# Optimization experiments

Measured on AMD Instinct MI355X. Metric: run time of the kernel, lower is better.

Reference implementation:

```python
import jax, jax.numpy as jnp
import numpy as np

D_MODEL = 1024
N_HEAD = 16
ATT_DIM = D_MODEL // N_HEAD  # 64
B, S = 8, 2048


def setup_inputs() -> dict:
    key = jax.random.key(0)
    kq, kk, kv, kwq, kwk, kwv = jax.random.split(key, 6)
    # xavier_uniform bound for Linear(hidden_dim -> att_dim)
    bound = float(np.sqrt(6.0 / (D_MODEL + ATT_DIM)))
    return {
        "q": jax.random.normal(kq, (B, S, D_MODEL), dtype=jnp.float32),
        "k": jax.random.normal(kk, (B, S, D_MODEL), dtype=jnp.float32),
        "v": jax.random.normal(kv, (B, S, D_MODEL), dtype=jnp.float32),
        "Wq": jax.random.uniform(kwq, (ATT_DIM, D_MODEL), jnp.float32, -bound, bound),
        "Wk": jax.random.uniform(kwk, (ATT_DIM, D_MODEL), jnp.float32, -bound, bound),
        "Wv": jax.random.uniform(kwv, (ATT_DIM, D_MODEL), jnp.float32, -bound, bound),
    }


def reference(q, k, v, Wq, Wk, Wv):
    # Linear projections (no bias): [B,S,d_model] @ [d_model,att_dim]
    qp = jnp.einsum('bsd,ed->bse', q, Wq)
    kp = jnp.einsum('bsd,ed->bse', k, Wk)
    vp = jnp.einsum('bsd,ed->bse', v, Wv)
    # Scores: note original divides by att_dim (not sqrt)
    scores = jnp.einsum('bqe,bke->bqk', qp, kp) / ATT_DIM
    probs = jax.nn.softmax(scores, axis=-1)  # [B,S,S]
    att = jnp.einsum('bqk,bke->bqe', probs, vp)  # [B,S,att_dim]
    # dropout is identity in eval mode
    return (att, probs)
```

## Files before the change

### kernel.cpp

```cpp
#include <hip/hip_runtime.h>
#include <hip/hip_bf16.h>

#define D_MODEL 1024
#define ATT_DIM 64
#define BATCH 8
#define SEQ 2048
#define MROWS (BATCH * SEQ)

typedef short bf16x8 __attribute__((ext_vector_type(8)));
typedef float f32x4 __attribute__((ext_vector_type(4)));
typedef long lx2 __attribute__((ext_vector_type(2)));

#define MFMA16(a, b, c) __builtin_amdgcn_mfma_f32_16x16x32_bf16((a), (b), (c), 0, 0, 0)

__device__ inline short f2bf(float f) {
    union { __hip_bfloat16 h; short s; } u;
    u.h = __float2bfloat16(f);
    return u.s;
}

__device__ __forceinline__ unsigned cvtpk(float lo, float hi) {
    unsigned r;
    asm("v_cvt_pk_bf16_f32 %0, %1, %2" : "=v"(r) : "v"(lo), "v"(hi));
    return r;
}

__device__ __forceinline__ void gload_lds16(const float* g, float* l) {
    __builtin_amdgcn_global_load_lds(
        (const __attribute__((address_space(1))) void*)g,
        (__attribute__((address_space(3))) void*)l, 16, 0, 0);
}

__global__ __launch_bounds__(256) void wcvt_kernel(
    const float* __restrict__ Wq, const float* __restrict__ Wk,
    const float* __restrict__ Wv, short* __restrict__ Wbf)
{
    const int idx = blockIdx.x * 256 + threadIdx.x;
    const int per = ATT_DIM * D_MODEL;
    const int base = idx * 8;
    const int mi = base / per;
    const int off = base - mi * per;
    const float* src = (mi == 0) ? Wq : (mi == 1 ? Wk : Wv);
    const float sc = (mi == 0) ? (1.0f / 64.0f) : 1.0f;
    const float4 a = *reinterpret_cast<const float4*>(src + off);
    const float4 b = *reinterpret_cast<const float4*>(src + off + 4);
    bf16x8 r;
    r[0] = f2bf(a.x * sc); r[1] = f2bf(a.y * sc);
    r[2] = f2bf(a.z * sc); r[3] = f2bf(a.w * sc);
    r[4] = f2bf(b.x * sc); r[5] = f2bf(b.y * sc);
    r[6] = f2bf(b.z * sc); r[7] = f2bf(b.w * sc);
    *reinterpret_cast<bf16x8*>(Wbf + base) = r;
}

__global__ __launch_bounds__(256) void proj_mfma_kernel(
    const float* __restrict__ q, const float* __restrict__ k,
    const float* __restrict__ v, const short* __restrict__ Wbf,
    short* __restrict__ qp, short* __restrict__ kp, short* __restrict__ vpT)
{
    const int mat = blockIdx.y;
    const float* x = (mat == 0) ? q : (mat == 1 ? k : v);
    const short* W = Wbf + mat * ATT_DIM * D_MODEL;

    __shared__ float As[2][4096];

    const int tid = threadIdx.x;
    const int w = tid >> 6;
    const int l = tid & 63;
    const int lr = l & 15;
    const int g = l >> 4;

    const int m0 = blockIdx.x * 64;
    const int row = w * 16 + lr;
    const int xr = (row & 7) << 4;

    f32x4 acc[4] = {};

    #define STAGE(c, buf)                                                      \
        {                                                                      \
            const int kt_ = (c) * 64;                                          \
            _Pragma("unroll")                                                  \
            for (int j = 0; j < 4; ++j) {                                      \
                const int rs = (w * 4 + j) * 4 + g;                            \
                const int scb = (lr * 16) ^ ((rs & 7) << 4);                   \
                gload_lds16(x + (long)(m0 + rs) * D_MODEL + kt_ + (scb >> 2),  \
                            &As[buf][(w * 4 + j) * 256]);                      \
            }                                                                  \
        }

    #define WFRAG(c, ks, ef)                                                   \
        (*reinterpret_cast<const bf16x8*>(                                     \
            W + ((ef) * 16 + lr) * D_MODEL + (c) * 64 + (ks) * 32 + g * 8))

    bf16x8 wreg[8];
    #pragma unroll
    for (int ks = 0; ks < 2; ++ks)
        #pragma unroll
        for (int ef = 0; ef < 4; ++ef) wreg[ks * 4 + ef] = WFRAG(0, ks, ef);

    STAGE(0, 0);
    __syncthreads();

    for (int c = 0; c < 16; ++c) {
        const int buf = c & 1;
        bf16x8 wnext[8];
        if (c < 15) {
            STAGE(c + 1, buf ^ 1);
            #pragma unroll
            for (int ks = 0; ks < 2; ++ks)
                #pragma unroll
                for (int ef = 0; ef < 4; ++ef)
                    wnext[ks * 4 + ef] = WFRAG(c + 1, ks, ef);
        }

        const char* Ab = (const char*)&As[buf][0] + row * 256;
        #pragma unroll
        for (int ks = 0; ks < 2; ++ks) {
            const int b0 = ks * 128 + g * 32;
            const float4 a0 = *reinterpret_cast<const float4*>(Ab + (b0 ^ xr));
            const float4 a1 = *reinterpret_cast<const float4*>(Ab + ((b0 + 16) ^ xr));
            bf16x8 af;
            af[0] = f2bf(a0.x); af[1] = f2bf(a0.y); af[2] = f2bf(a0.z); af[3] = f2bf(a0.w);
            af[4] = f2bf(a1.x); af[5] = f2bf(a1.y); af[6] = f2bf(a1.z); af[7] = f2bf(a1.w);
            #pragma unroll
            for (int ef = 0; ef < 4; ++ef)
                acc[ef] = MFMA16(af, wreg[ks * 4 + ef], acc[ef]);
        }
        __syncthreads();
        if (c < 15) {
            #pragma unroll
            for (int i = 0; i < 8; ++i) wreg[i] = wnext[i];
        }
    }
    #undef STAGE
    #undef WFRAG

    if (mat < 2) {
        short* out = (mat == 0) ? qp : kp;
        #pragma unroll
        for (int ef = 0; ef < 4; ++ef)
            #pragma unroll
            for (int j = 0; j < 4; ++j)
                out[(long)(m0 + w * 16 + g * 4 + j) * ATT_DIM + ef * 16 + lr] =
                    f2bf(acc[ef][j]);
    } else {
        const int b = m0 / SEQ;
        const int s0 = (m0 - b * SEQ) + w * 16;
        #pragma unroll
        for (int ef = 0; ef < 4; ++ef)
            #pragma unroll
            for (int j = 0; j < 4; ++j)
                vpT[((long)b * ATT_DIM + ef * 16 + lr) * SEQ + s0 + g * 4 + j] =
                    f2bf(acc[ef][j]);
    }
}

union AttnSmem {
    short pk[8][16][40];
    float o[8][64][17];
};

__global__ __launch_bounds__(512) void attn_kernel(
    const short* __restrict__ qp, const short* __restrict__ kp,
    const short* __restrict__ vpT, float* __restrict__ probs,
    float* __restrict__ att)
{
    __shared__ __align__(16) AttnSmem u;
    __shared__ float stats_m[8][16];
    __shared__ float stats_l[8][16];

    const int tid = threadIdx.x;
    const int w = tid >> 6;
    const int l = tid & 63;
    const int lr = l & 15;
    const int g = l >> 4;

    const int b = blockIdx.y;
    const int q0 = blockIdx.x * 16;

    const short* qpb = qp + ((long)b * SEQ + q0) * ATT_DIM;
    const short* kpb = kp + (long)b * SEQ * ATT_DIM;
    const short* vTb = vpT + (long)b * ATT_DIM * SEQ;

    const bf16x8 qa0 = *reinterpret_cast<const bf16x8*>(qpb + lr * ATT_DIM + g * 8);
    const bf16x8 qa1 = *reinterpret_cast<const bf16x8*>(qpb + lr * ATT_DIM + 32 + g * 8);

    const int kbeg = w * 256;

    f32x4 s[8][2];
    #pragma unroll
    for (int ch = 0; ch < 8; ++ch) {
        const short* kb = kpb + (long)(kbeg + ch * 32) * ATT_DIM;
        const bf16x8 kb00 = *reinterpret_cast<const bf16x8*>(kb + lr * ATT_DIM + g * 8);
        const bf16x8 kb01 = *reinterpret_cast<const bf16x8*>(kb + lr * ATT_DIM + 32 + g * 8);
        const bf16x8 kb10 = *reinterpret_cast<const bf16x8*>(kb + (16 + lr) * ATT_DIM + g * 8);
        const bf16x8 kb11 = *reinterpret_cast<const bf16x8*>(kb + (16 + lr) * ATT_DIM + 32 + g * 8);
        f32x4 t0 = {}; t0 = MFMA16(kb00, qa0, t0); t0 = MFMA16(kb01, qa1, t0);
        f32x4 t1 = {}; t1 = MFMA16(kb10, qa0, t1); t1 = MFMA16(kb11, qa1, t1);
        s[ch][0] = t0; s[ch][1] = t1;
    }

    float mw = -1e30f;
    #pragma unroll
    for (int ch = 0; ch < 8; ++ch)
        #pragma unroll
        for (int h = 0; h < 2; ++h)
            mw = fmaxf(mw, fmaxf(fmaxf(s[ch][h][0], s[ch][h][1]),
                                 fmaxf(s[ch][h][2], s[ch][h][3])));
    mw = fmaxf(mw, __shfl_xor(mw, 16));
    mw = fmaxf(mw, __shfl_xor(mw, 32));

    float lw = 0.f;
    #pragma unroll
    for (int ch = 0; ch < 8; ++ch)
        #pragma unroll
        for (int h = 0; h < 2; ++h)
            #pragma unroll
            for (int j = 0; j < 4; ++j) {
                const float e = __expf(s[ch][h][j] - mw);
                s[ch][h][j] = e;
                lw += e;
            }
    lw += __shfl_xor(lw, 16);
    lw += __shfl_xor(lw, 32);

    if (l < 16) { stats_m[w][l] = mw; stats_l[w][l] = lw; }
    __syncthreads();

    float gm = stats_m[0][lr];
    #pragma unroll
    for (int ww = 1; ww < 8; ++ww) gm = fmaxf(gm, stats_m[ww][lr]);
    float tot = 0.f;
    #pragma unroll
    for (int ww = 0; ww < 8; ++ww)
        tot += stats_l[ww][lr] * __expf(stats_m[ww][lr] - gm);
    const float scale = __expf(mw - gm) / tot;
    #pragma unroll
    for (int ch = 0; ch < 8; ++ch)
        #pragma unroll
        for (int h = 0; h < 2; ++h)
            s[ch][h] *= scale;

    f32x4 accO[4] = {};
    float* pbase = probs + ((long)b * SEQ + q0 + lr) * SEQ;

    #pragma unroll
    for (int ch = 0; ch < 8; ++ch) {
        const int k0 = kbeg + ch * 32;
        *reinterpret_cast<f32x4*>(pbase + k0 + g * 4)      = s[ch][0];
        *reinterpret_cast<f32x4*>(pbase + k0 + 16 + g * 4) = s[ch][1];

        uint4 cc;
        cc.x = cvtpk(s[ch][0][0], s[ch][0][1]);
        cc.y = cvtpk(s[ch][0][2], s[ch][0][3]);
        cc.z = cvtpk(s[ch][1][0], s[ch][1][1]);
        cc.w = cvtpk(s[ch][1][2], s[ch][1][3]);
        *reinterpret_cast<uint4*>(&u.pk[w][lr][g * 8]) = cc;

        const long lo = *reinterpret_cast<const long*>(
            &u.pk[w][lr][(2 * (g & 1)) * 8 + (g >> 1) * 4]);
        const long hi = *reinterpret_cast<const long*>(
            &u.pk[w][lr][(2 * (g & 1) + 1) * 8 + (g >> 1) * 4]);
        union { lx2 l2; bf16x8 v; } pbu;
        pbu.l2[0] = lo; pbu.l2[1] = hi;
        const bf16x8 pb = pbu.v;

        #pragma unroll
        for (int ef = 0; ef < 4; ++ef) {
            const bf16x8 va = *reinterpret_cast<const bf16x8*>(
                vTb + (long)(ef * 16 + lr) * SEQ + k0 + g * 8);
            accO[ef] = MFMA16(va, pb, accO[ef]);
        }
    }

    __syncthreads();
    #pragma unroll
    for (int ef = 0; ef < 4; ++ef)
        #pragma unroll
        for (int j = 0; j < 4; ++j)
            u.o[w][ef * 16 + g * 4 + j][lr] = accO[ef][j];
    __syncthreads();

    {
        const int qr = tid >> 5;
        const int e0 = (tid & 31) * 2;
        float o0 = 0.f, o1 = 0.f;
        #pragma unroll
        for (int ww = 0; ww < 8; ++ww) {
            o0 += u.o[ww][e0][qr];
            o1 += u.o[ww][e0 + 1][qr];
        }
        float2 o = make_float2(o0, o1);
        *reinterpret_cast<float2*>(att + ((long)b * SEQ + q0 + qr) * ATT_DIM + e0) = o;
    }
}

extern "C" void kernel_launch(void* const* d_in, const int* in_sizes, int n_in,
                              void* d_out, int out_size, void* d_ws, size_t ws_size,
                              hipStream_t stream)
{
    const float* q  = (const float*)d_in[0];
    const float* k  = (const float*)d_in[1];
    const float* v  = (const float*)d_in[2];
    const float* Wq = (const float*)d_in[3];
    const float* Wk = (const float*)d_in[4];
    const float* Wv = (const float*)d_in[5];

    float* att   = (float*)d_out;
    float* probs = att + (size_t)BATCH * SEQ * ATT_DIM;

    short* qp  = (short*)d_ws;
    short* kp  = qp + (size_t)MROWS * ATT_DIM;
    short* vpT = kp + (size_t)MROWS * ATT_DIM;
    short* Wbf = vpT + (size_t)MROWS * ATT_DIM;

    wcvt_kernel<<<dim3(96), 256, 0, stream>>>(Wq, Wk, Wv, Wbf);

    proj_mfma_kernel<<<dim3(MROWS / 64, 3), 256, 0, stream>>>(
        q, k, v, Wbf, qp, kp, vpT);

    attn_kernel<<<dim3(SEQ / 16, BATCH), 512, 0, stream>>>(
        qp, kp, vpT, probs, att);
}
```

Before: 151.2 us.

## Split attention key range across 16 waves and load W fragments in-loop

```diff
diff --git a/kernel.cpp b/kernel.cpp
--- a/kernel.cpp
+++ b/kernel.cpp
@@ -87,31 +87,14 @@
             }                                                                  \
         }
 
-    #define WFRAG(c, ks, ef)                                                   \
-        (*reinterpret_cast<const bf16x8*>(                                     \
-            W + ((ef) * 16 + lr) * D_MODEL + (c) * 64 + (ks) * 32 + g * 8))
-
-    bf16x8 wreg[8];
-    #pragma unroll
-    for (int ks = 0; ks < 2; ++ks)
-        #pragma unroll
-        for (int ef = 0; ef < 4; ++ef) wreg[ks * 4 + ef] = WFRAG(0, ks, ef);
-
     STAGE(0, 0);
     __syncthreads();
 
     for (int c = 0; c < 16; ++c) {
         const int buf = c & 1;
-        bf16x8 wnext[8];
-        if (c < 15) {
-            STAGE(c + 1, buf ^ 1);
-            #pragma unroll
-            for (int ks = 0; ks < 2; ++ks)
-                #pragma unroll
-                for (int ef = 0; ef < 4; ++ef)
-                    wnext[ks * 4 + ef] = WFRAG(c + 1, ks, ef);
-        }
-
+        if (c < 15) STAGE(c + 1, buf ^ 1);
+
+        const int kt = c * 64;
         const char* Ab = (const char*)&As[buf][0] + row * 256;
         #pragma unroll
         for (int ks = 0; ks < 2; ++ks) {
@@ -122,17 +105,15 @@
             af[0] = f2bf(a0.x); af[1] = f2bf(a0.y); af[2] = f2bf(a0.z); af[3] = f2bf(a0.w);
             af[4] = f2bf(a1.x); af[5] = f2bf(a1.y); af[6] = f2bf(a1.z); af[7] = f2bf(a1.w);
             #pragma unroll
-            for (int ef = 0; ef < 4; ++ef)
-                acc[ef] = MFMA16(af, wreg[ks * 4 + ef], acc[ef]);
+            for (int ef = 0; ef < 4; ++ef) {
+                const bf16x8 wf = *reinterpret_cast<const bf16x8*>(
+                    W + (ef * 16 + lr) * D_MODEL + kt + ks * 32 + g * 8);
+                acc[ef] = MFMA16(af, wf, acc[ef]);
+            }
         }
         __syncthreads();
-        if (c < 15) {
-            #pragma unroll
-            for (int i = 0; i < 8; ++i) wreg[i] = wnext[i];
-        }
     }
     #undef STAGE
-    #undef WFRAG
 
     if (mat < 2) {
         short* out = (mat == 0) ? qp : kp;
@@ -155,18 +136,20 @@
 }
 
 union AttnSmem {
-    short pk[8][16][40];
-    float o[8][64][17];
+    struct {
+        short pk[16][16][40];
+        float m[16][16];
+        float l[16][16];
+    } a;
+    float o[16][64][17];
 };
 
-__global__ __launch_bounds__(512) void attn_kernel(
+__global__ __launch_bounds__(1024) void attn_kernel(
     const short* __restrict__ qp, const short* __restrict__ kp,
     const short* __restrict__ vpT, float* __restrict__ probs,
     float* __restrict__ att)
 {
     __shared__ __align__(16) AttnSmem u;
-    __shared__ float stats_m[8][16];
-    __shared__ float stats_l[8][16];
 
     const int tid = threadIdx.x;
     const int w = tid >> 6;
@@ -184,11 +167,11 @@
     const bf16x8 qa0 = *reinterpret_cast<const bf16x8*>(qpb + lr * ATT_DIM + g * 8);
     const bf16x8 qa1 = *reinterpret_cast<const bf16x8*>(qpb + lr * ATT_DIM + 32 + g * 8);
 
-    const int kbeg = w * 256;
-
-    f32x4 s[8][2];
-    #pragma unroll
-    for (int ch = 0; ch < 8; ++ch) {
+    const int kbeg = w * 128;
+
+    f32x4 s[4][2];
+    #pragma unroll
+    for (int ch = 0; ch < 4; ++ch) {
         const short* kb = kpb + (long)(kbeg + ch * 32) * ATT_DIM;
         const bf16x8 kb00 = *reinterpret_cast<const bf16x8*>(kb + lr * ATT_DIM + g * 8);
         const bf16x8 kb01 = *reinterpret_cast<const bf16x8*>(kb + lr * ATT_DIM + 32 + g * 8);
@@ -201,7 +184,7 @@
 
     float mw = -1e30f;
     #pragma unroll
-    for (int ch = 0; ch < 8; ++ch)
+    for (int ch = 0; ch < 4; ++ch)
         #pragma unroll
         for (int h = 0; h < 2; ++h)
             mw = fmaxf(mw, fmaxf(fmaxf(s[ch][h][0], s[ch][h][1]),
@@ -211,7 +194,7 @@
 
     float lw = 0.f;
     #pragma unroll
-    for (int ch = 0; ch < 8; ++ch)
+    for (int ch = 0; ch < 4; ++ch)
         #pragma unroll
         for (int h = 0; h < 2; ++h)
             #pragma unroll
@@ -223,19 +206,19 @@
     lw += __shfl_xor(lw, 16);
     lw += __shfl_xor(lw, 32);
 
-    if (l < 16) { stats_m[w][l] = mw; stats_l[w][l] = lw; }
+    if (l < 16) { u.a.m[w][l] = mw; u.a.l[w][l] = lw; }
     __syncthreads();
 
-    float gm = stats_m[0][lr];
-    #pragma unroll
-    for (int ww = 1; ww < 8; ++ww) gm = fmaxf(gm, stats_m[ww][lr]);
+    float gm = u.a.m[0][lr];
+    #pragma unroll
+    for (int ww = 1; ww < 16; ++ww) gm = fmaxf(gm, u.a.m[ww][lr]);
     float tot = 0.f;
     #pragma unroll
-    for (int ww = 0; ww < 8; ++ww)
-        tot += stats_l[ww][lr] * __expf(stats_m[ww][lr] - gm);
+    for (int ww = 0; ww < 16; ++ww)
+        tot += u.a.l[ww][lr] * __expf(u.a.m[ww][lr] - gm);
     const float scale = __expf(mw - gm) / tot;
     #pragma unroll
-    for (int ch = 0; ch < 8; ++ch)
+    for (int ch = 0; ch < 4; ++ch)
         #pragma unroll
         for (int h = 0; h < 2; ++h)
             s[ch][h] *= scale;
@@ -244,7 +227,7 @@
     float* pbase = probs + ((long)b * SEQ + q0 + lr) * SEQ;
 
     #pragma unroll
-    for (int ch = 0; ch < 8; ++ch) {
+    for (int ch = 0; ch < 4; ++ch) {
         const int k0 = kbeg + ch * 32;
         *reinterpret_cast<f32x4*>(pbase + k0 + g * 4)      = s[ch][0];
         *reinterpret_cast<f32x4*>(pbase + k0 + 16 + g * 4) = s[ch][1];
@@ -254,12 +237,12 @@
         cc.y = cvtpk(s[ch][0][2], s[ch][0][3]);
         cc.z = cvtpk(s[ch][1][0], s[ch][1][1]);
         cc.w = cvtpk(s[ch][1][2], s[ch][1][3]);
-        *reinterpret_cast<uint4*>(&u.pk[w][lr][g * 8]) = cc;
+        *reinterpret_cast<uint4*>(&u.a.pk[w][lr][g * 8]) = cc;
 
         const long lo = *reinterpret_cast<const long*>(
-            &u.pk[w][lr][(2 * (g & 1)) * 8 + (g >> 1) * 4]);
+            &u.a.pk[w][lr][(2 * (g & 1)) * 8 + (g >> 1) * 4]);
         const long hi = *reinterpret_cast<const long*>(
-            &u.pk[w][lr][(2 * (g & 1) + 1) * 8 + (g >> 1) * 4]);
+            &u.a.pk[w][lr][(2 * (g & 1) + 1) * 8 + (g >> 1) * 4]);
         union { lx2 l2; bf16x8 v; } pbu;
         pbu.l2[0] = lo; pbu.l2[1] = hi;
         const bf16x8 pb = pbu.v;
@@ -281,16 +264,12 @@
     __syncthreads();
 
     {
-        const int qr = tid >> 5;
-        const int e0 = (tid & 31) * 2;
-        float o0 = 0.f, o1 = 0.f;
-        #pragma unroll
-        for (int ww = 0; ww < 8; ++ww) {
-            o0 += u.o[ww][e0][qr];
-            o1 += u.o[ww][e0 + 1][qr];
-        }
-        float2 o = make_float2(o0, o1);
-        *reinterpret_cast<float2*>(att + ((long)b * SEQ + q0 + qr) * ATT_DIM + e0) = o;
+        const int qr = tid >> 6;
+        const int e0 = tid & 63;
+        float oacc = 0.f;
+        #pragma unroll
+        for (int ww = 0; ww < 16; ++ww) oacc += u.o[ww][e0][qr];
+        att[((long)b * SEQ + q0 + qr) * ATT_DIM + e0] = oacc;
     }
 }
 
@@ -318,6 +297,6 @@
     proj_mfma_kernel<<<dim3(MROWS / 64, 3), 256, 0, stream>>>(
         q, k, v, Wbf, qp, kp, vpT);
 
-    attn_kernel<<<dim3(SEQ / 16, BATCH), 512, 0, stream>>>(
+    attn_kernel<<<dim3(SEQ / 16, BATCH), 1024, 0, stream>>>(
         qp, kp, vpT, probs, att);
 }
```

After: 153.2 us. About the same (+1.3%).
